# Kernel optimization log

Measured on AMD Instinct MI355X. Metric: run time of the kernel, lower is better.

The kernel has to match this reference:

```python
import jax, jax.numpy as jnp
import numpy as np

N = 100000      # nodes
E = 1600000     # edges (avg degree 16)
IN_DIM = 16
D = 128         # layer width
H = 2           # attention heads (GATLayer default n_heads=2)
FC = 128
OUT_DIM = 4
L = 2           # len(layer_channels)-1 attention layers


def _gat_layer(x, src, dst, Wk, bk, Wq, bq, Wv, bv):
    # x: [N, D]; src/dst: [E]
    n = x.shape[0]
    dk = D // H
    k = (x @ Wk + bk).reshape(n, H, dk)
    q = (x @ Wq + bq).reshape(n, H, dk)
    v = (x @ Wv + bv).reshape(n, H, dk)
    # per-edge score: k_src . q_dst  -> [E, H]
    score = jnp.einsum('ehd,ehd->eh', k[src], q[dst])
    # edge softmax grouped by destination node
    smax = jax.ops.segment_max(score, dst, num_segments=n)          # [N, H]
    ex = jnp.exp(score - smax[dst])                                 # [E, H]
    denom = jax.ops.segment_sum(ex, dst, num_segments=n)           # [N, H]
    attn = ex / denom[dst]                                          # [E, H]
    # weighted scatter-sum of source values to destinations
    msg = v[src] * attn[:, :, None]                                 # [E, H, dk]
    res = jax.ops.segment_sum(msg, dst, num_segments=n)             # [N, H, dk]
    return res.reshape(n, D)


def setup_inputs() -> dict:
    key = jax.random.key(0)
    ks = jax.random.split(key, 24)
    def lin(k, fin, fout):
        w = jax.random.normal(k, (fin, fout), jnp.float32) * (1.0 / np.sqrt(fin))
        return w
    inp = {}
    inp['x'] = jax.random.normal(ks[0], (N, IN_DIM), jnp.float32)
    inp['src'] = jax.random.randint(ks[1], (E,), 0, N, jnp.int32)
    inp['dst'] = jax.random.randint(ks[2], (E,), 0, N, jnp.int32)
    inp['fc0_w'] = lin(ks[3], IN_DIM, D)
    inp['fc0_b'] = jnp.zeros((D,), jnp.float32)
    inp['Wk'] = jnp.stack([lin(ks[4 + i], D, D) for i in range(L)])
    inp['bk'] = jnp.zeros((L, D), jnp.float32)
    inp['Wq'] = jnp.stack([lin(ks[6 + i], D, D) for i in range(L)])
    inp['bq'] = jnp.zeros((L, D), jnp.float32)
    inp['Wv'] = jnp.stack([lin(ks[8 + i], D, D) for i in range(L)])
    inp['bv'] = jnp.zeros((L, D), jnp.float32)
    inp['ws_w'] = jnp.stack([lin(ks[10 + i], D, D) for i in range(L)])
    inp['ws_b'] = jnp.zeros((L, D), jnp.float32)
    inp['fc1_w'] = lin(ks[12], D, FC)
    inp['fc1_b'] = jnp.zeros((FC,), jnp.float32)
    inp['fc2_w'] = lin(ks[13], FC, OUT_DIM)
    inp['fc2_b'] = jnp.zeros((OUT_DIM,), jnp.float32)
    return inp


def reference(x, src, dst, fc0_w, fc0_b, Wk, bk, Wq, bq, Wv, bv, ws_w, ws_b, fc1_w, fc1_b, fc2_w, fc2_b):
    h = x @ fc0_w + fc0_b                                           # [N, D]
    for i in range(L):
        h = (h @ ws_w[i] + ws_b[i]) + _gat_layer(h, src, dst, Wk[i], bk[i], Wq[i], bq[i], Wv[i], bv[i])
        if i != L - 1:
            h = jax.nn.gelu(h)
    h = jax.nn.gelu(h @ fc1_w + fc1_b)                              # fc_channels > 0 branch
    return h @ fc2_w + fc2_b                                        # [N, OUT_DIM]
```

## Files before the change

### kernel.cpp

```cpp
#include <hip/hip_runtime.h>
#include <math.h>


typedef _Float16 f16x8 __attribute__((ext_vector_type(8)));
typedef _Float16 h2 __attribute__((ext_vector_type(2)));
typedef float f32x4 __attribute__((ext_vector_type(4)));

__device__ __forceinline__ ushort f2h(float x) {
    union { _Float16 h; ushort u; } v;
    v.h = (_Float16)x;
    return v.u;
}

__device__ __forceinline__ float gelu_f(float x) {
    float y = 0.7978845608028654f * (x + 0.044715f * x * x * x);
    float t = __expf(2.f * y);
    return x * t / (t + 1.f);
}

__device__ __forceinline__ h2 pk2(float a, float b) {
    return __builtin_bit_cast(h2, __builtin_amdgcn_cvt_pkrtz(a, b));
}

__global__ void k_hist(const int* __restrict__ dst, int* __restrict__ deg,
                       int* __restrict__ rank, int e) {
    int i = blockIdx.x * blockDim.x + threadIdx.x;
    if (i < e) rank[i] = atomicAdd(&deg[dst[i]], 1);
}

__global__ __launch_bounds__(256) void k_part(const int* __restrict__ deg,
                                              int* __restrict__ pre,
                                              int* __restrict__ bsum, int n) {
    __shared__ int lds[256];
    int t = threadIdx.x;
    int base = blockIdx.x * 1024 + t * 4;
    int d0 = 0, d1 = 0, d2 = 0, d3 = 0;
    if (base + 3 < n) {
        int4 d = *(const int4*)&deg[base];
        d0 = d.x; d1 = d.y; d2 = d.z; d3 = d.w;
    } else {
        if (base + 0 < n) d0 = deg[base + 0];
        if (base + 1 < n) d1 = deg[base + 1];
        if (base + 2 < n) d2 = deg[base + 2];
        if (base + 3 < n) d3 = deg[base + 3];
    }
    int s0 = d0, s1 = s0 + d1, s2 = s1 + d2, s3 = s2 + d3;
    lds[t] = s3;
    __syncthreads();
    for (int off = 1; off < 256; off <<= 1) {
        int v = (t >= off) ? lds[t - off] : 0;
        __syncthreads();
        lds[t] += v;
        __syncthreads();
    }
    int excl = lds[t] - s3;
    if (base + 0 < n) pre[base + 0] = excl;
    if (base + 1 < n) pre[base + 1] = excl + s0;
    if (base + 2 < n) pre[base + 2] = excl + s1;
    if (base + 3 < n) pre[base + 3] = excl + s2;
    if (t == 255) bsum[blockIdx.x] = lds[255];
}

__global__ void k_scanb(int* __restrict__ bsum, int nb) {
    __shared__ int lds[128];
    int t = threadIdx.x;
    int v = (t < nb) ? bsum[t] : 0;
    lds[t] = v;
    __syncthreads();
    for (int off = 1; off < 128; off <<= 1) {
        int u = (t >= off) ? lds[t - off] : 0;
        __syncthreads();
        lds[t] += u;
        __syncthreads();
    }
    if (t < nb) bsum[t] = lds[t] - v;
}

__global__ __launch_bounds__(256) void k_add(int* __restrict__ rowp,
                                             const int* __restrict__ bsum, int n,
                                             int e) {
    int t = threadIdx.x;
    int base = blockIdx.x * 1024 + t * 4;
    int off = bsum[blockIdx.x];
#pragma unroll
    for (int j = 0; j < 4; ++j) {
        int i = base + j;
        if (i < n) rowp[i] += off;
    }
    if (blockIdx.x == 0 && t == 0) rowp[n] = e;
}

__global__ void k_scatter(const int* __restrict__ src, const int* __restrict__ dst,
                          const int* __restrict__ rank, const int* __restrict__ rowp,
                          int* __restrict__ csrc, int e) {
    int i = blockIdx.x * blockDim.x + threadIdx.x;
    if (i < e) csrc[rowp[dst[i]] + rank[i]] = src[i];
}

__global__ void k_pack(const float* __restrict__ Wk, const float* __restrict__ Wq,
                       const float* __restrict__ Wv, const float* __restrict__ Ws,
                       const float* __restrict__ Wfc1, ushort* __restrict__ Wp) {
    int id = blockIdx.y;
    const float* src;
    if (id < 8) {
        int m = id & 3, layer = id >> 2;
        src = (m == 0) ? Wk : (m == 1) ? Wq : (m == 2) ? Wv : Ws;
        src += layer * 16384;
    } else {
        src = Wfc1;
    }
    int o = blockIdx.x * 256 + threadIdx.x;
    int j = o & 7, l = (o >> 3) & 63, nf = (o >> 9) & 7, kc = o >> 12;
    int row = kc * 32 + ((l >> 4) << 3) + j;
    int col = nf * 16 + (l & 15);
    Wp[id * 16384 + o] = f2h(src[row * 128 + col]);
}

__device__ __forceinline__ void stage_Ah(const ushort* __restrict__ A, int n,
                                         int rbase, char* Asb, int t) {
#pragma unroll
    for (int i = 0; i < 4; ++i) {
        int b = t * 16 + i * 4096;
        int r = b >> 8;
        uint4 v = {0u, 0u, 0u, 0u};
        if (rbase + r < n)
            v = *(const uint4*)((const char*)A + (size_t)rbase * 256 + b);
        *(uint4*)(Asb + (b ^ ((r & 7) << 4))) = v;
    }
}

__global__ __launch_bounds__(256) void k_gemm_proj(
    const ushort* __restrict__ A, int n, const ushort* __restrict__ Wp,
    const float* __restrict__ b0, ushort* __restrict__ o0, int ostr0,
    const float* __restrict__ b1, ushort* __restrict__ o1, int ostr1,
    const float* __restrict__ b2_, ushort* __restrict__ o2, int ostr2,
    const float* __restrict__ b3, ushort* __restrict__ o3, int ostr3,
    const float* __restrict__ X0, const float* __restrict__ W0,
    const float* __restrict__ B0, int fc0mode) {
    __shared__ ushort As[64 * 128];
    __shared__ ushort Ws[16384];
    char* Asb = (char*)As;
    int t = threadIdx.x;
    int rbase = blockIdx.x * 64;

    const uint4* wsrc = (const uint4*)Wp;
    uint4 wreg[8];
#pragma unroll
    for (int i = 0; i < 8; ++i) wreg[i] = wsrc[t + i * 256];

    if (fc0mode) {
        float* WT  = (float*)Ws;
        float* bi0 = WT + 2048;
        float* xs  = bi0 + 128;
#pragma unroll
        for (int i = 0; i < 8; ++i) {
            int idx = t * 8 + i;
            WT[idx] = W0[(idx & 15) * 128 + (idx >> 4)];
        }
        if (t < 128) bi0[t] = B0[t];
        {
            int row = t >> 2, k0 = (t & 3) * 4;
            float4 xv = {0.f, 0.f, 0.f, 0.f};
            if (rbase + row < n)
                xv = *(const float4*)&X0[(size_t)(rbase + row) * 16 + k0];
            *(float4*)&xs[row * 16 + k0] = xv;
        }
        __syncthreads();
        int row = t >> 2;
        float x[16];
#pragma unroll
        for (int i = 0; i < 4; ++i)
            *(float4*)&x[i * 4] = *(const float4*)&xs[row * 16 + i * 4];
        int cbase = (t & 3) * 32;
        for (int c = cbase; c < cbase + 32; ++c) {
            const float4* wc = (const float4*)&WT[c * 16];
            float4 wa = wc[0], wb = wc[1], wd = wc[2], we = wc[3];
            float acc = bi0[c];
            acc += x[0] * wa.x + x[1] * wa.y + x[2] * wa.z + x[3] * wa.w;
            acc += x[4] * wb.x + x[5] * wb.y + x[6] * wb.z + x[7] * wb.w;
            acc += x[8] * wd.x + x[9] * wd.y + x[10] * wd.z + x[11] * wd.w;
            acc += x[12] * we.x + x[13] * we.y + x[14] * we.z + x[15] * we.w;
            int b = (row * 256 + c * 2) ^ ((row & 7) << 4);
            *(ushort*)(Asb + b) = f2h(acc);
        }
    } else {
        stage_Ah(A, n, rbase, Asb, t);
    }
    __syncthreads();

    int w = t >> 6, l = t & 63;
    int arow = w * 16 + (l & 15);
    int kq = l >> 4;

    f16x8 a[4];
#pragma unroll
    for (int kc = 0; kc < 4; ++kc) {
        int byte = (arow * 256 + kc * 64 + kq * 16) ^ ((arow & 7) << 4);
        a[kc] = *(const f16x8*)(Asb + byte);
    }
    __syncthreads();

    for (int m = 0; m < 4; ++m) {
#pragma unroll
        for (int i = 0; i < 8; ++i) ((uint4*)Ws)[t + i * 256] = wreg[i];
        __syncthreads();

        if (m < 3) {
#pragma unroll
            for (int i = 0; i < 8; ++i)
                wreg[i] = wsrc[(m + 1) * 2048 + t + i * 256];
        }

        const float* bias; ushort* op; int ostr;
        if (m == 0)      { bias = b0; op = o0; ostr = ostr0; }
        else if (m == 1) { bias = b1; op = o1; ostr = ostr1; }
        else if (m == 2) { bias = b2_; op = o2; ostr = ostr2; }
        else             { bias = b3; op = o3; ostr = ostr3; }

        f32x4 acc[8];
#pragma unroll
        for (int nf = 0; nf < 8; ++nf) acc[nf] = (f32x4){0.f, 0.f, 0.f, 0.f};

#pragma unroll
        for (int kc = 0; kc < 4; ++kc) {
#pragma unroll
            for (int nf = 0; nf < 8; ++nf) {
                f16x8 b = *(const f16x8*)(Ws + (((kc * 8 + nf) * 64 + l) << 3));
                acc[nf] = __builtin_amdgcn_mfma_f32_16x16x32_f16(a[kc], b, acc[nf], 0, 0, 0);
            }
        }
        __syncthreads();

#pragma unroll
        for (int nf = 0; nf < 8; ++nf) {
            int col = nf * 16 + (l & 15);
            float bia = bias[col];
#pragma unroll
            for (int r = 0; r < 4; ++r) {
                int row = w * 16 + (l >> 4) * 4 + r;
                int b = (row * 256 + col * 2) ^ ((row & 7) << 4);
                *(ushort*)(Asb + b) = f2h(acc[nf][r] + bia);
            }
        }
        __syncthreads();

#pragma unroll
        for (int i = 0; i < 4; ++i) {
            int b = t * 16 + i * 4096;
            int r = b >> 8, c = b & 255;
            uint4 v = *(const uint4*)(Asb + (b ^ ((r & 7) << 4)));
            if (rbase + r < n)
                *(uint4*)((char*)op + (size_t)(rbase + r) * ostr * 2 + c) = v;
        }
    }
}

__global__ __launch_bounds__(256) void k_gemm_fc(
    const ushort* __restrict__ A, int n, const ushort* __restrict__ Wp,
    const float* __restrict__ bias1, const float* __restrict__ W2,
    const float* __restrict__ bias2, float* __restrict__ out2) {
    __shared__ ushort As[64 * 128];
    __shared__ ushort Ws[16384];
    char* Asb = (char*)As;
    int t = threadIdx.x;
    int rbase = blockIdx.x * 64;

    stage_Ah(A, n, rbase, Asb, t);

    const uint4* wsrc = (const uint4*)Wp;
#pragma unroll
    for (int i = 0; i < 8; ++i) ((uint4*)Ws)[t + i * 256] = wsrc[t + i * 256];

    __syncthreads();

    int w = t >> 6, l = t & 63;
    int arow = w * 16 + (l & 15);
    int kq = l >> 4;

    f16x8 a[4];
#pragma unroll
    for (int kc = 0; kc < 4; ++kc) {
        int byte = (arow * 256 + kc * 64 + kq * 16) ^ ((arow & 7) << 4);
        a[kc] = *(const f16x8*)(Asb + byte);
    }

    f32x4 acc[8];
#pragma unroll
    for (int nf = 0; nf < 8; ++nf) acc[nf] = (f32x4){0.f, 0.f, 0.f, 0.f};

#pragma unroll
    for (int kc = 0; kc < 4; ++kc) {
#pragma unroll
        for (int nf = 0; nf < 8; ++nf) {
            f16x8 b = *(const f16x8*)(Ws + (((kc * 8 + nf) * 64 + l) << 3));
            acc[nf] = __builtin_amdgcn_mfma_f32_16x16x32_f16(a[kc], b, acc[nf], 0, 0, 0);
        }
    }

    float pj[4][4];
#pragma unroll
    for (int r = 0; r < 4; ++r)
#pragma unroll
        for (int j = 0; j < 4; ++j) pj[r][j] = 0.f;
#pragma unroll
    for (int nf = 0; nf < 8; ++nf) {
        int col = nf * 16 + (l & 15);
        float4 w2v = *(const float4*)&W2[col * 4];
        float bia = bias1[col];
#pragma unroll
        for (int r = 0; r < 4; ++r) {
            float o = gelu_f(acc[nf][r] + bia);
            pj[r][0] += o * w2v.x;
            pj[r][1] += o * w2v.y;
            pj[r][2] += o * w2v.z;
            pj[r][3] += o * w2v.w;
        }
    }
#pragma unroll
    for (int off = 1; off < 16; off <<= 1)
#pragma unroll
        for (int r = 0; r < 4; ++r)
#pragma unroll
            for (int j = 0; j < 4; ++j)
                pj[r][j] += __shfl_xor(pj[r][j], off);
    int jj = l & 15;
    if (jj < 4) {
#pragma unroll
        for (int r = 0; r < 4; ++r) {
            int row = rbase + w * 16 + (l >> 4) * 4 + r;
            if (row < n) {
                float v = (jj == 0) ? pj[r][0] : (jj == 1) ? pj[r][1]
                        : (jj == 2) ? pj[r][2] : pj[r][3];
                out2[(size_t)row * 4 + jj] = v + bias2[jj];
            }
        }
    }
}

__global__ void k_edge_hf(const ushort* __restrict__ KV, const ushort* __restrict__ Q,
                          const int* __restrict__ rowp, const int* __restrict__ csrc,
                          ushort* __restrict__ H, int n, int act) {
    int wid = (int)((blockIdx.x * blockDim.x + threadIdx.x) >> 6);
    int lane = threadIdx.x & 63;
    if (wid >= n) return;
    int qb = lane >> 4;
    unsigned fb = (lane & 15) * 8u;
    int e0 = rowp[wid], e1 = rowp[wid + 1];

    uint4 qr = *(const uint4*)(Q + (((unsigned)wid << 7) + fb));
    h2 q0 = __builtin_bit_cast(h2, qr.x), q1 = __builtin_bit_cast(h2, qr.y);
    h2 q2 = __builtin_bit_cast(h2, qr.z), q3 = __builtin_bit_cast(h2, qr.w);

    float m = -1e30f, denom = 0.f;
    h2 hz = {(_Float16)0.f, (_Float16)0.f};
    h2 acc0 = hz, acc1 = hz, acc2 = hz, acc3 = hz;

#define EDGE_BODY(KR, VR, VALID)                                               \
    {                                                                          \
        float sc = __builtin_amdgcn_fdot2(__builtin_bit_cast(h2, KR.x), q0,    \
                   __builtin_amdgcn_fdot2(__builtin_bit_cast(h2, KR.y), q1,    \
                   __builtin_amdgcn_fdot2(__builtin_bit_cast(h2, KR.z), q2,    \
                   __builtin_amdgcn_fdot2(__builtin_bit_cast(h2, KR.w), q3,    \
                                          0.f, false), false), false), false); \
        sc += __shfl_xor(sc, 1);                                               \
        sc += __shfl_xor(sc, 2);                                               \
        sc += __shfl_xor(sc, 4);                                               \
        if (VALID && sc > m + 4.f) {                                           \
            float ss = __expf(m - sc);                                         \
            m = sc;                                                            \
            denom *= ss;                                                       \
            h2 hs = pk2(ss, ss);                                               \
            acc0 *= hs; acc1 *= hs; acc2 *= hs; acc3 *= hs;                    \
        }                                                                      \
        float p = VALID ? __expf(sc - m) : 0.f;                                \
        denom += p;                                                            \
        h2 hp = pk2(p, p);                                                     \
        acc0 = __builtin_bit_cast(h2, VR.x) * hp + acc0;                       \
        acc1 = __builtin_bit_cast(h2, VR.y) * hp + acc1;                       \
        acc2 = __builtin_bit_cast(h2, VR.z) * hp + acc2;                       \
        acc3 = __builtin_bit_cast(h2, VR.w) * hp + acc3;                       \
    }

    for (int eb = e0; eb < e1; eb += 64) {
        int cnt = min(64, e1 - eb);
        int sl = (eb + lane < e1) ? csrc[eb + lane] : 0;
        int nq = (cnt + 3) >> 2;
        for (int c0 = 0; c0 < nq; c0 += 4) {
            int ei0 = (c0 + 0) * 4 + qb, ei1 = (c0 + 1) * 4 + qb;
            int ei2 = (c0 + 2) * 4 + qb, ei3 = (c0 + 3) * 4 + qb;
            bool v0 = ei0 < cnt, v1 = ei1 < cnt, v2 = ei2 < cnt, v3 = ei3 < cnt;
            unsigned of0 = (((unsigned)__shfl(sl, ei0 & 63)) << 8) + fb;
            unsigned of1 = (((unsigned)__shfl(sl, ei1 & 63)) << 8) + fb;
            unsigned of2 = (((unsigned)__shfl(sl, ei2 & 63)) << 8) + fb;
            unsigned of3 = (((unsigned)__shfl(sl, ei3 & 63)) << 8) + fb;
            uint4 kr0 = *(const uint4*)(KV + of0);
            uint4 vr0 = *(const uint4*)(KV + of0 + 128);
            uint4 kr1 = *(const uint4*)(KV + of1);
            uint4 vr1 = *(const uint4*)(KV + of1 + 128);
            uint4 kr2 = *(const uint4*)(KV + of2);
            uint4 vr2 = *(const uint4*)(KV + of2 + 128);
            uint4 kr3 = *(const uint4*)(KV + of3);
            uint4 vr3 = *(const uint4*)(KV + of3 + 128);
            EDGE_BODY(kr0, vr0, v0);
            if (v1 || c0 + 4 < nq) EDGE_BODY(kr1, vr1, v1);
            if (v2 || c0 + 4 < nq) EDGE_BODY(kr2, vr2, v2);
            if (v3 || c0 + 4 < nq) EDGE_BODY(kr3, vr3, v3);
        }
    }
#undef EDGE_BODY

#pragma unroll
    for (int dist = 16; dist <= 32; dist <<= 1) {
        float mo = __shfl_xor(m, dist);
        float dn = __shfl_xor(denom, dist);
        unsigned w0 = __shfl_xor(__builtin_bit_cast(unsigned, acc0), dist);
        unsigned w1 = __shfl_xor(__builtin_bit_cast(unsigned, acc1), dist);
        unsigned w2 = __shfl_xor(__builtin_bit_cast(unsigned, acc2), dist);
        unsigned w3 = __shfl_xor(__builtin_bit_cast(unsigned, acc3), dist);
        float mn = fmaxf(m, mo);
        float sA = __expf(m - mn), sB = __expf(mo - mn);
        denom = denom * sA + dn * sB;
        h2 hA = pk2(sA, sA), hB = pk2(sB, sB);
        acc0 = acc0 * hA + __builtin_bit_cast(h2, w0) * hB;
        acc1 = acc1 * hA + __builtin_bit_cast(h2, w1) * hB;
        acc2 = acc2 * hA + __builtin_bit_cast(h2, w2) * hB;
        acc3 = acc3 * hA + __builtin_bit_cast(h2, w3) * hB;
        m = mn;
    }

    if (lane < 16) {
        float inv = (denom > 0.f) ? 1.f / denom : 0.f;
        ushort* hp = H + (((unsigned)wid << 7) + fb);
        uint4 hr = *(const uint4*)hp;
        h2 s0 = __builtin_bit_cast(h2, hr.x), s1 = __builtin_bit_cast(h2, hr.y);
        h2 s2 = __builtin_bit_cast(h2, hr.z), s3 = __builtin_bit_cast(h2, hr.w);
        float o0 = (float)s0.x + (float)acc0.x * inv;
        float o1 = (float)s0.y + (float)acc0.y * inv;
        float o2 = (float)s1.x + (float)acc1.x * inv;
        float o3 = (float)s1.y + (float)acc1.y * inv;
        float o4 = (float)s2.x + (float)acc2.x * inv;
        float o5 = (float)s2.y + (float)acc2.y * inv;
        float o6 = (float)s3.x + (float)acc3.x * inv;
        float o7 = (float)s3.y + (float)acc3.y * inv;
        if (act) {
            o0 = gelu_f(o0); o1 = gelu_f(o1); o2 = gelu_f(o2); o3 = gelu_f(o3);
            o4 = gelu_f(o4); o5 = gelu_f(o5); o6 = gelu_f(o6); o7 = gelu_f(o7);
        }
        uint4 o;
        o.x = __builtin_bit_cast(unsigned, pk2(o0, o1));
        o.y = __builtin_bit_cast(unsigned, pk2(o2, o3));
        o.z = __builtin_bit_cast(unsigned, pk2(o4, o5));
        o.w = __builtin_bit_cast(unsigned, pk2(o6, o7));
        *(uint4*)hp = o;
    }
}

extern "C" void kernel_launch(void* const* d_in, const int* in_sizes, int n_in,
                              void* d_out, int out_size, void* d_ws, size_t ws_size,
                              hipStream_t stream) {
    const float* x     = (const float*)d_in[0];
    const int*   src   = (const int*)d_in[1];
    const int*   dst   = (const int*)d_in[2];
    const float* fc0_w = (const float*)d_in[3];
    const float* fc0_b = (const float*)d_in[4];
    const float* Wk    = (const float*)d_in[5];
    const float* bk    = (const float*)d_in[6];
    const float* Wq    = (const float*)d_in[7];
    const float* bq    = (const float*)d_in[8];
    const float* Wv    = (const float*)d_in[9];
    const float* bv    = (const float*)d_in[10];
    const float* ws_w  = (const float*)d_in[11];
    const float* ws_b  = (const float*)d_in[12];
    const float* fc1_w = (const float*)d_in[13];
    const float* fc1_b = (const float*)d_in[14];
    const float* fc2_w = (const float*)d_in[15];
    const float* fc2_b = (const float*)d_in[16];

    int n = in_sizes[0] / 16;
    int e = in_sizes[1];

    ushort* hA  = (ushort*)d_ws;
    ushort* hB  = hA + (size_t)n * 128;
    ushort* KV  = hB + (size_t)n * 128;
    ushort* Qb  = KV + (size_t)n * 256;
    ushort* Wp  = Qb + (size_t)n * 128;
    int* deg    = (int*)(Wp + 9 * 16384);
    int* rowp   = deg + n;
    int* csrc   = rowp + n + 1;
    int* rank   = csrc + e;
    int* bsum   = rank + e;

    int nb = (n + 1023) / 1024;

    hipMemsetAsync(deg, 0, (size_t)n * sizeof(int), stream);
    k_hist<<<(e + 255) / 256, 256, 0, stream>>>(dst, deg, rank, e);
    k_part<<<nb, 256, 0, stream>>>(deg, rowp, bsum, n);
    k_scanb<<<1, 128, 0, stream>>>(bsum, nb);
    k_add<<<nb, 256, 0, stream>>>(rowp, bsum, n, e);
    k_scatter<<<(e + 255) / 256, 256, 0, stream>>>(src, dst, rank, rowp, csrc, e);

    k_pack<<<dim3(64, 9), 256, 0, stream>>>(Wk, Wq, Wv, ws_w, fc1_w, Wp);

    int gx = (n + 63) / 64;
    k_gemm_proj<<<gx, 256, 0, stream>>>(nullptr, n, Wp, bk, KV, 256, bq, Qb, 128,
                                        bv, KV + 128, 256, ws_b, hB, 128,
                                        x, fc0_w, fc0_b, 1);
    k_edge_hf<<<(n + 3) / 4, 256, 0, stream>>>(KV, Qb, rowp, csrc, hB, n, 1);
    k_gemm_proj<<<gx, 256, 0, stream>>>(hB, n, Wp + 4 * 16384, bk + 128, KV, 256,
                                        bq + 128, Qb, 128, bv + 128, KV + 128, 256,
                                        ws_b + 128, hA, 128,
                                        nullptr, nullptr, nullptr, 0);
    k_edge_hf<<<(n + 3) / 4, 256, 0, stream>>>(KV, Qb, rowp, csrc, hA, n, 0);

    k_gemm_fc<<<gx, 256, 0, stream>>>(hA, n, Wp + 8 * 16384, fc1_b, fc2_w, fc2_b,
                                      (float*)d_out);
}
```

Before: 525.7 us.

## Map four destination nodes per wavefront in edge attention kernel

The edge aggregation kernel now assigns one 16-lane group per destination node, so each wavefront handles four nodes instead of splitting one node's edges across four quarter-waves. This removes the cross-group online-softmax merge through shuffles and the idle lanes during the final write. The cost is divergence: each wave loops to the maximum degree among its four nodes, and with degree about 16 that leaves fewer independent gathers in flight per node. The grid shrinks fourfold to match.

```diff
diff --git a/kernel.cpp b/kernel.cpp
--- a/kernel.cpp
+++ b/kernel.cpp
@@ -340,14 +340,21 @@
 __global__ void k_edge_hf(const ushort* __restrict__ KV, const ushort* __restrict__ Q,
                           const int* __restrict__ rowp, const int* __restrict__ csrc,
                           ushort* __restrict__ H, int n, int act) {
-    int wid = (int)((blockIdx.x * blockDim.x + threadIdx.x) >> 6);
+    int wave = (int)((blockIdx.x * blockDim.x + threadIdx.x) >> 6);
     int lane = threadIdx.x & 63;
-    if (wid >= n) return;
-    int qb = lane >> 4;
-    unsigned fb = (lane & 15) * 8u;
-    int e0 = rowp[wid], e1 = rowp[wid + 1];
-
-    uint4 qr = *(const uint4*)(Q + (((unsigned)wid << 7) + fb));
+    int g = lane >> 4, lg = lane & 15;
+    int wid = wave * 4 + g;
+    bool active = wid < n;
+    int e0 = active ? rowp[wid] : 0;
+    int e1 = active ? rowp[wid + 1] : 0;
+    int myE = e1 - e0;
+    int maxE = myE;
+    maxE = max(maxE, __shfl_xor(maxE, 16));
+    maxE = max(maxE, __shfl_xor(maxE, 32));
+    unsigned fb = lg * 8u;
+
+    uint4 qr = {0u, 0u, 0u, 0u};
+    if (active) qr = *(const uint4*)(Q + (((unsigned)wid << 7) + fb));
     h2 q0 = __builtin_bit_cast(h2, qr.x), q1 = __builtin_bit_cast(h2, qr.y);
     h2 q2 = __builtin_bit_cast(h2, qr.z), q3 = __builtin_bit_cast(h2, qr.w);
 
@@ -381,54 +388,27 @@
         acc3 = __builtin_bit_cast(h2, VR.w) * hp + acc3;                       \
     }
 
-    for (int eb = e0; eb < e1; eb += 64) {
-        int cnt = min(64, e1 - eb);
-        int sl = (eb + lane < e1) ? csrc[eb + lane] : 0;
-        int nq = (cnt + 3) >> 2;
-        for (int c0 = 0; c0 < nq; c0 += 4) {
-            int ei0 = (c0 + 0) * 4 + qb, ei1 = (c0 + 1) * 4 + qb;
-            int ei2 = (c0 + 2) * 4 + qb, ei3 = (c0 + 3) * 4 + qb;
-            bool v0 = ei0 < cnt, v1 = ei1 < cnt, v2 = ei2 < cnt, v3 = ei3 < cnt;
-            unsigned of0 = (((unsigned)__shfl(sl, ei0 & 63)) << 8) + fb;
-            unsigned of1 = (((unsigned)__shfl(sl, ei1 & 63)) << 8) + fb;
-            unsigned of2 = (((unsigned)__shfl(sl, ei2 & 63)) << 8) + fb;
-            unsigned of3 = (((unsigned)__shfl(sl, ei3 & 63)) << 8) + fb;
-            uint4 kr0 = *(const uint4*)(KV + of0);
-            uint4 vr0 = *(const uint4*)(KV + of0 + 128);
-            uint4 kr1 = *(const uint4*)(KV + of1);
-            uint4 vr1 = *(const uint4*)(KV + of1 + 128);
-            uint4 kr2 = *(const uint4*)(KV + of2);
-            uint4 vr2 = *(const uint4*)(KV + of2 + 128);
-            uint4 kr3 = *(const uint4*)(KV + of3);
-            uint4 vr3 = *(const uint4*)(KV + of3 + 128);
-            EDGE_BODY(kr0, vr0, v0);
-            if (v1 || c0 + 4 < nq) EDGE_BODY(kr1, vr1, v1);
-            if (v2 || c0 + 4 < nq) EDGE_BODY(kr2, vr2, v2);
-            if (v3 || c0 + 4 < nq) EDGE_BODY(kr3, vr3, v3);
+    for (int eb = 0; eb < maxE; eb += 16) {
+        int sl = (eb + lg < myE) ? csrc[e0 + eb + lg] : 0;
+        int cnt = myE - eb;
+        int jmax = min(16, maxE - eb);
+        for (int j = 0; j < jmax; j += 2) {
+            bool vA = j < cnt, vB = (j + 1) < cnt;
+            int sA = __shfl(sl, (lane & 48) + j);
+            int sB = __shfl(sl, (lane & 48) + ((j + 1) & 15));
+            unsigned ofA = (((unsigned)sA) << 8) + fb;
+            unsigned ofB = (((unsigned)sB) << 8) + fb;
+            uint4 kA = *(const uint4*)(KV + ofA);
+            uint4 vA4 = *(const uint4*)(KV + ofA + 128);
+            uint4 kB = *(const uint4*)(KV + ofB);
+            uint4 vB4 = *(const uint4*)(KV + ofB + 128);
+            EDGE_BODY(kA, vA4, vA);
+            EDGE_BODY(kB, vB4, vB);
         }
     }
 #undef EDGE_BODY
 
-#pragma unroll
-    for (int dist = 16; dist <= 32; dist <<= 1) {
-        float mo = __shfl_xor(m, dist);
-        float dn = __shfl_xor(denom, dist);
-        unsigned w0 = __shfl_xor(__builtin_bit_cast(unsigned, acc0), dist);
-        unsigned w1 = __shfl_xor(__builtin_bit_cast(unsigned, acc1), dist);
-        unsigned w2 = __shfl_xor(__builtin_bit_cast(unsigned, acc2), dist);
-        unsigned w3 = __shfl_xor(__builtin_bit_cast(unsigned, acc3), dist);
-        float mn = fmaxf(m, mo);
-        float sA = __expf(m - mn), sB = __expf(mo - mn);
-        denom = denom * sA + dn * sB;
-        h2 hA = pk2(sA, sA), hB = pk2(sB, sB);
-        acc0 = acc0 * hA + __builtin_bit_cast(h2, w0) * hB;
-        acc1 = acc1 * hA + __builtin_bit_cast(h2, w1) * hB;
-        acc2 = acc2 * hA + __builtin_bit_cast(h2, w2) * hB;
-        acc3 = acc3 * hA + __builtin_bit_cast(h2, w3) * hB;
-        m = mn;
-    }
-
-    if (lane < 16) {
+    if (active) {
         float inv = (denom > 0.f) ? 1.f / denom : 0.f;
         ushort* hp = H + (((unsigned)wid << 7) + fb);
         uint4 hr = *(const uint4*)hp;
@@ -502,15 +482,16 @@
     k_pack<<<dim3(64, 9), 256, 0, stream>>>(Wk, Wq, Wv, ws_w, fc1_w, Wp);
 
     int gx = (n + 63) / 64;
+    int ge = (n + 15) / 16;
     k_gemm_proj<<<gx, 256, 0, stream>>>(nullptr, n, Wp, bk, KV, 256, bq, Qb, 128,
                                         bv, KV + 128, 256, ws_b, hB, 128,
                                         x, fc0_w, fc0_b, 1);
-    k_edge_hf<<<(n + 3) / 4, 256, 0, stream>>>(KV, Qb, rowp, csrc, hB, n, 1);
+    k_edge_hf<<<ge, 256, 0, stream>>>(KV, Qb, rowp, csrc, hB, n, 1);
     k_gemm_proj<<<gx, 256, 0, stream>>>(hB, n, Wp + 4 * 16384, bk + 128, KV, 256,
                                         bq + 128, Qb, 128, bv + 128, KV + 128, 256,
                                         ws_b + 128, hA, 128,
                                         nullptr, nullptr, nullptr, 0);
-    k_edge_hf<<<(n + 3) / 4, 256, 0, stream>>>(KV, Qb, rowp, csrc, hA, n, 0);
+    k_edge_hf<<<ge, 256, 0, stream>>>(KV, Qb, rowp, csrc, hA, n, 0);
 
     k_gemm_fc<<<gx, 256, 0, stream>>>(hA, n, Wp + 8 * 16384, fc1_b, fc2_w, fc2_b,
                                       (float*)d_out);
```

New measurement: 536.7 us. +2.1%, slower.
